# Kernel optimization log

Measured on AMD Instinct MI355X. Metric: run time of the kernel, lower is better.

## Reference

```python
import jax, jax.numpy as jnp
import numpy as np

# Config: b=2, n=1024, dim=512, heads=8, dim_head=64, L=8 slices/head, temperature=0.1

def setup_inputs() -> dict:
    key = jax.random.key(0)
    ks = jax.random.split(key, 5)
    b, n, dim = 2, 1024, 512
    heads, dim_head, L = 8, 64, 8
    inner = heads * dim_head
    x = jax.random.normal(ks[0], (b, n, dim), jnp.float32)
    W_qkv = jax.random.normal(ks[1], (dim, 3 * inner), jnp.float32) * 0.02
    theta = jax.random.normal(ks[2], (heads, L, dim_head), jnp.float32)
    W_out = jax.random.normal(ks[3], (inner, dim), jnp.float32) * 0.02
    b_out = jnp.zeros((dim,), jnp.float32)
    return {"x": x, "W_qkv": W_qkv, "theta": theta, "W_out": W_out, "b_out": b_out}


def reference(x, W_qkv, theta, W_out, b_out):
    b, n, dim = x.shape
    heads, L, dim_head = theta.shape
    scale = dim_head ** -0.5
    temperature = 0.1
    # QKV projection (no bias) and head split: b n (h d) -> b h n d
    qkv = x @ W_qkv
    q, k, v = jnp.split(qkv, 3, axis=-1)
    sh = lambda t: t.reshape(b, n, heads, dim_head).transpose(0, 2, 1, 3)
    q = sh(q) * scale
    k = sh(k) * scale
    v = sh(v)
    # Esp: learnable unit slice directions per head, 1D projections
    th = theta / jnp.linalg.norm(theta, axis=-1, keepdims=True)  # [h, L, d]
    qp = jnp.einsum('bhnd,hld->bhln', q, th)  # [b,h,L,n]
    kp = jnp.einsum('bhnd,hld->bhln', k, th)
    # per-slice soft 1D transport plan (rows sum to 1), averaged over slices,
    # scaled to total-mass-1 plan (rows sum 1/n)
    d2 = (qp[..., :, None] - kp[..., None, :]) ** 2  # [b,h,L,n,n]
    plans = jax.nn.softmax(-d2 / temperature, axis=-1)
    P = plans.mean(axis=2) / n  # [b,h,n,n], rows sum to 1/n
    # SA: attn = attn * attn.shape[-1] -> row-stochastic
    attn = P * n
    out = jnp.einsum('bhnm,bhmd->bhnd', attn, v)
    out = out.transpose(0, 2, 1, 3).reshape(b, n, heads * dim_head)
    out = out @ W_out + b_out  # to_out Linear (dropout=0 in eval)
    return out, attn
```

## Files before the change

### kernel.cpp

```cpp
#include <hip/hip_runtime.h>
#include <hip/hip_bf16.h>

#define CEXP (-14.4269504088896340736f)

typedef __attribute__((ext_vector_type(8))) short bfrag8;
typedef __attribute__((ext_vector_type(4))) float fvec4;
typedef __attribute__((ext_vector_type(8))) unsigned short ushort8;

__device__ inline unsigned short f2bf(float f) {
    unsigned u = __builtin_bit_cast(unsigned, f);
    u += 0x7fffu + ((u >> 16) & 1u);
    return (unsigned short)(u >> 16);
}
__device__ inline float bf2f(unsigned short h) {
    unsigned u = ((unsigned)h) << 16;
    return __builtin_bit_cast(float, u);
}

template <int CTRL, int RMASK>
__device__ __forceinline__ float dpp_add(float v) {
    int m = __builtin_amdgcn_update_dpp(0, __builtin_bit_cast(int, v), CTRL, RMASK, 0xf, true);
    return v + __builtin_bit_cast(float, m);
}
__device__ __forceinline__ float wave_sum64(float v) {
    v = dpp_add<0xB1,  0xf>(v);
    v = dpp_add<0x4E,  0xf>(v);
    v = dpp_add<0x141, 0xf>(v);
    v = dpp_add<0x140, 0xf>(v);
    v = dpp_add<0x142, 0xa>(v);
    v = dpp_add<0x143, 0xc>(v);
    return __builtin_bit_cast(float, __builtin_amdgcn_readlane(__builtin_bit_cast(int, v), 63));
}

__global__ __launch_bounds__(256) void k_wproj(const float* __restrict__ Wqkv,
                                               const float* __restrict__ theta,
                                               float* __restrict__ Wqp,
                                               float* __restrict__ Wkp,
                                               float* __restrict__ Wv) {
    __shared__ float th_s[64 * 65];
    int tid = threadIdx.x;
    int hl = tid & 63, cl = tid >> 6;
    #pragma unroll
    for (int i = 0; i < 16; ++i) {
        int r = cl * 16 + i;
        th_s[r * 65 + hl] = theta[r * 64 + hl];
    }
    __syncthreads();
    const float* ts = th_s + hl * 65;
    float ss = 0.f;
    #pragma unroll 8
    for (int d = 0; d < 64; ++d) ss = fmaf(ts[d], ts[d], ss);
    float inv = rsqrtf(ss);
    int c = blockIdx.x * 4 + cl;
    int h = hl >> 3;
    const float* wq = Wqkv + c * 1536 + h * 64;
    const float* wk = wq + 512;
    float aq = 0.f, ak = 0.f;
    #pragma unroll 4
    for (int d = 0; d < 64; ++d) {
        float tv = ts[d];
        aq = fmaf(wq[d], tv, aq);
        ak = fmaf(wk[d], tv, ak);
    }
    Wqp[c * 64 + hl] = aq * inv;
    Wkp[c * 64 + hl] = ak * inv;

    int c0 = blockIdx.x * 4;
    const float4* src = (const float4*)(Wqkv + 1024);
    float4* dst = (float4*)Wv;
    #pragma unroll
    for (int j = 0; j < 2; ++j) {
        int idx = j * 256 + tid;
        int cr = c0 + (idx >> 7), o4 = idx & 127;
        dst[cr * 128 + o4] = src[cr * 384 + o4];
    }
}

__global__ __launch_bounds__(512) void k_qkp(const float* __restrict__ x,
                                             const float* __restrict__ Wqp,
                                             const float* __restrict__ Wkp,
                                             float* __restrict__ qp,
                                             float* __restrict__ kp) {
    __shared__ float xs[4 * 512];
    __shared__ float comb[4][128][4];
    int tid = threadIdx.x;
    int i0 = blockIdx.x * 4;
    const float4* xg = (const float4*)(x + i0 * 512);
    ((float4*)xs)[tid] = xg[tid];
    __syncthreads();

    int t  = tid & 127;
    int kh = tid >> 7;
    int hl = t & 63;
    const float* Bm = (t & 64) ? Wkp : Wqp;
    float a[4] = {0.f, 0.f, 0.f, 0.f};
    int c4b = kh * 32;
    for (int c4 = c4b; c4 < c4b + 32; ++c4) {
        float b0 = Bm[(c4 * 4 + 0) * 64 + hl];
        float b1 = Bm[(c4 * 4 + 1) * 64 + hl];
        float b2 = Bm[(c4 * 4 + 2) * 64 + hl];
        float b3 = Bm[(c4 * 4 + 3) * 64 + hl];
        #pragma unroll
        for (int r = 0; r < 4; ++r) {
            float4 xv = *(const float4*)(xs + r * 512 + c4 * 4);
            a[r] = fmaf(xv.x, b0, fmaf(xv.y, b1, fmaf(xv.z, b2, fmaf(xv.w, b3, a[r]))));
        }
    }
    #pragma unroll
    for (int r = 0; r < 4; ++r) comb[kh][t][r] = a[r];
    __syncthreads();

    if (tid < 128) {
        int hl2 = tid & 63;
        int h = hl2 >> 3, l = hl2 & 7;
        float* dst = (tid & 64) ? kp : qp;
        int b = i0 >> 10, i = i0 & 1023;
        fvec4 st;
        #pragma unroll
        for (int r = 0; r < 4; ++r)
            st[r] = (comb[0][tid][r] + comb[1][tid][r] + comb[2][tid][r] + comb[3][tid][r]) * 0.125f;
        *(fvec4*)(dst + ((b * 8 + h) * 8 + l) * 1024 + i) = st;
    }
}

__global__ __launch_bounds__(256) void k_vproj(const float* __restrict__ x,
                                               const float* __restrict__ Wv,
                                               unsigned short* __restrict__ vThi,
                                               unsigned short* __restrict__ vTlo) {
    __shared__ float xs[8 * 512];
    __shared__ float comb[2][128][8];
    int tid = threadIdx.x;
    int blk = blockIdx.x;
    int cs = blk & 3;
    int i0 = (blk >> 2) * 8;
    const float4* xg = (const float4*)(x + i0 * 512);
    float4* xs4 = (float4*)xs;
    #pragma unroll
    for (int j = 0; j < 4; ++j) xs4[j * 256 + tid] = xg[j * 256 + tid];
    __syncthreads();

    int t  = tid & 127;
    int kh = tid >> 7;
    int col = cs * 128 + t;
    const float* wp = Wv + col;
    float a[8];
    #pragma unroll
    for (int r = 0; r < 8; ++r) a[r] = 0.f;
    int c4b = kh * 64;
    for (int c4 = c4b; c4 < c4b + 64; ++c4) {
        float w0 = wp[(c4 * 4 + 0) * 512];
        float w1 = wp[(c4 * 4 + 1) * 512];
        float w2 = wp[(c4 * 4 + 2) * 512];
        float w3 = wp[(c4 * 4 + 3) * 512];
        #pragma unroll
        for (int r = 0; r < 8; ++r) {
            float4 xv = *(const float4*)(xs + r * 512 + c4 * 4);
            a[r] = fmaf(xv.x, w0, fmaf(xv.y, w1, fmaf(xv.z, w2, fmaf(xv.w, w3, a[r]))));
        }
    }
    #pragma unroll
    for (int r = 0; r < 8; ++r) comb[kh][t][r] = a[r];
    __syncthreads();

    if (tid < 128) {
        int col2 = cs * 128 + tid;
        int h = col2 >> 6, d = col2 & 63;
        int b = i0 >> 10, ib = i0 & 1023;
        ushort8 vh, vl;
        #pragma unroll
        for (int r = 0; r < 8; ++r) {
            float v = comb[0][tid][r] + comb[1][tid][r];
            unsigned short hi = f2bf(v);
            vh[r] = hi;
            vl[r] = f2bf(v - bf2f(hi));
        }
        size_t off = (size_t)(b * 8 + h) * 65536 + (size_t)d * 1024 + ib;
        *(ushort8*)(vThi + off) = vh;
        *(ushort8*)(vTlo + off) = vl;
    }
}

__global__ __launch_bounds__(512) void k_attn_pv(const float* __restrict__ qp,
                                                 const float* __restrict__ kp,
                                                 const unsigned short* __restrict__ vThi,
                                                 const unsigned short* __restrict__ vTlo,
                                                 float* __restrict__ attn,
                                                 float* __restrict__ oh) {
    __shared__ float s_buf[8 * 1024];
    __shared__ float sc[4 * 64 * 4];
    int bx = blockIdx.x;
    int idx = bx >> 3;
    int bh = (bx & 7) * 2 + (idx >> 7);
    int rowbase = (idx & 127) * 8;
    int tid = threadIdx.x;
    int w = tid >> 6, lane = tid & 63;

    const float4* kp4 = (const float4*)(kp + bh * 8192);
    float4* kps4 = (float4*)s_buf;
    #pragma unroll
    for (int k = 0; k < 4; ++k) kps4[k * 512 + tid] = kp4[k * 512 + tid];

    int r = rowbase + w;
    float qv[8];
    #pragma unroll
    for (int l = 0; l < 8; ++l) qv[l] = qp[bh * 8192 + l * 1024 + r];
    __syncthreads();

    const fvec4 CE = {CEXP, CEXP, CEXP, CEXP};
    fvec4 acc4[4];
    #pragma unroll
    for (int mm = 0; mm < 4; ++mm) acc4[mm] = (fvec4){0.f, 0.f, 0.f, 0.f};

    for (int l = 0; l < 8; ++l) {
        fvec4 kv4[4], e4[4];
        #pragma unroll
        for (int mm = 0; mm < 4; ++mm)
            kv4[mm] = *(const fvec4*)(s_buf + l * 1024 + mm * 256 + lane * 4);
        float sqs = -2.f * CEXP * qv[l];
        fvec4 sq4 = {sqs, sqs, sqs, sqs};
        fvec4 sum4 = {0.f, 0.f, 0.f, 0.f};
        #pragma unroll
        for (int mm = 0; mm < 4; ++mm) {
            fvec4 k2 = (kv4[mm] * kv4[mm]) * CE;
            fvec4 t  = sq4 * kv4[mm] + k2;
            fvec4 e;
            e[0] = __builtin_amdgcn_exp2f(t[0]);
            e[1] = __builtin_amdgcn_exp2f(t[1]);
            e[2] = __builtin_amdgcn_exp2f(t[2]);
            e[3] = __builtin_amdgcn_exp2f(t[3]);
            e4[mm] = e;
            sum4 += e;
        }
        float s = (sum4[0] + sum4[1]) + (sum4[2] + sum4[3]);
        float inv = 0.125f * __builtin_amdgcn_rcpf(wave_sum64(s));
        fvec4 inv4 = {inv, inv, inv, inv};
        #pragma unroll
        for (int mm = 0; mm < 4; ++mm) acc4[mm] = e4[mm] * inv4 + acc4[mm];
    }

    __syncthreads();

    unsigned short* ps = (unsigned short*)s_buf;
    int swz = w << 3;
    #pragma unroll
    for (int mm = 0; mm < 4; ++mm) {
        #pragma unroll
        for (int jj = 0; jj < 4; ++jj) {
            int j = mm * 256 + lane * 4 + jj;
            float v = acc4[mm][jj];
            unsigned short hi = f2bf(v);
            ps[w * 1024 + (j ^ swz)]       = hi;
            ps[(w + 8) * 1024 + (j ^ swz)] = f2bf(v - bf2f(hi));
        }
    }
    __syncthreads();

    float* aR = attn + ((size_t)(bh * 1024 + r)) * 1024;
    #pragma unroll
    for (int mm = 0; mm < 4; ++mm)
        __builtin_nontemporal_store(acc4[mm], (fvec4*)(aR + mm * 256 + lane * 4));

    int n0 = (w & 3) * 16;
    int kh = w >> 2;
    int ar  = lane & 15;
    int asw = (ar & 7) << 3;
    int ak  = (lane >> 4) * 8;
    const unsigned short* ap = ps + ar * 1024;
    size_t boff = (size_t)bh * 65536 + (size_t)(n0 + (lane & 15)) * 1024 + ak;
    const unsigned short* bh_p = vThi + boff;
    const unsigned short* bl_p = vTlo + boff;
    fvec4 c2 = {0.f, 0.f, 0.f, 0.f};
    #pragma unroll 4
    for (int s = kh * 16; s < kh * 16 + 16; ++s) {
        bfrag8 a  = *(const bfrag8*)(ap + ((s * 32 + ak) ^ asw));
        bfrag8 vh = *(const bfrag8*)(bh_p + s * 32);
        bfrag8 vl = *(const bfrag8*)(bl_p + s * 32);
        c2 = __builtin_amdgcn_mfma_f32_16x16x32_bf16(a, vh, c2, 0, 0, 0);
        c2 = __builtin_amdgcn_mfma_f32_16x16x32_bf16(a, vl, c2, 0, 0, 0);
    }
    if (w >= 4) {
        #pragma unroll
        for (int q = 0; q < 4; ++q) sc[(w - 4) * 256 + lane * 4 + q] = c2[q];
    }
    __syncthreads();
    if (w < 4) {
        int b = bh >> 3, h = bh & 7;
        #pragma unroll
        for (int q = 0; q < 4; ++q) {
            float t = c2[q] + sc[w * 256 + lane * 4 + q];
            t += __shfl_xor(t, 32);
            if (lane < 32) {
                int row = rowbase + (lane >> 4) * 4 + q;
                oh[(b * 1024 + row) * 512 + h * 64 + n0 + (lane & 15)] = t;
            }
        }
    }
}

__global__ __launch_bounds__(256) void k_out(const float* __restrict__ oh,
                                             const float* __restrict__ Wout,
                                             const float* __restrict__ bout,
                                             float* __restrict__ out) {
    __shared__ float xs[8 * 512];
    __shared__ float comb[2][128][8];
    int tid = threadIdx.x;
    int blk = blockIdx.x;
    int cs = blk & 3;
    int i0 = (blk >> 2) * 8;
    const float4* xg = (const float4*)(oh + i0 * 512);
    float4* xs4 = (float4*)xs;
    #pragma unroll
    for (int j = 0; j < 4; ++j) xs4[j * 256 + tid] = xg[j * 256 + tid];
    __syncthreads();

    int t  = tid & 127;
    int kh = tid >> 7;
    int col = cs * 128 + t;
    const float* wp = Wout + col;
    float a[8];
    #pragma unroll
    for (int r = 0; r < 8; ++r) a[r] = 0.f;
    int c4b = kh * 64;
    for (int c4 = c4b; c4 < c4b + 64; ++c4) {
        float w0 = wp[(c4 * 4 + 0) * 512];
        float w1 = wp[(c4 * 4 + 1) * 512];
        float w2 = wp[(c4 * 4 + 2) * 512];
        float w3 = wp[(c4 * 4 + 3) * 512];
        #pragma unroll
        for (int r = 0; r < 8; ++r) {
            float4 xv = *(const float4*)(xs + r * 512 + c4 * 4);
            a[r] = fmaf(xv.x, w0, fmaf(xv.y, w1, fmaf(xv.z, w2, fmaf(xv.w, w3, a[r]))));
        }
    }
    #pragma unroll
    for (int r = 0; r < 8; ++r) comb[kh][t][r] = a[r];
    __syncthreads();

    if (tid < 128) {
        int col2 = cs * 128 + tid;
        float bias = bout[col2];
        #pragma unroll
        for (int r = 0; r < 8; ++r)
            out[(i0 + r) * 512 + col2] = comb[0][tid][r] + comb[1][tid][r] + bias;
    }
}

extern "C" void kernel_launch(void* const* d_in, const int* in_sizes, int n_in,
                              void* d_out, int out_size, void* d_ws, size_t ws_size,
                              hipStream_t stream) {
    const float* x     = (const float*)d_in[0];
    const float* Wqkv  = (const float*)d_in[1];
    const float* theta = (const float*)d_in[2];
    const float* Wout  = (const float*)d_in[3];
    const float* bout  = (const float*)d_in[4];

    float* out  = (float*)d_out;
    float* attn = out + 2 * 1024 * 512;

    float* ws  = (float*)d_ws;
    float* Wqp = ws;
    float* Wkp = ws + 32768;
    float* qp  = ws + 65536;
    float* kp  = ws + 196608;
    unsigned short* vThi = (unsigned short*)(ws + 327680);
    unsigned short* vTlo = (unsigned short*)(ws + 851968);
    float* oh   = ws + 1376256;
    float* Wv   = ws + 2424832;

    k_wproj   <<<128,  256, 0, stream>>>(Wqkv, theta, Wqp, Wkp, Wv);
    k_qkp     <<<512,  512, 0, stream>>>(x, Wqp, Wkp, qp, kp);
    k_vproj   <<<1024, 256, 0, stream>>>(x, Wv, vThi, vTlo);
    k_attn_pv <<<2048, 512, 0, stream>>>(qp, kp, vThi, vTlo, attn, oh);
    k_out     <<<1024, 256, 0, stream>>>(oh, Wout, bout, out);
}
```

Measured before the change: 138.1 us.

## Move output projection to split-bf16 MFMA with pre-transposed W_out

```diff
diff --git a/kernel.cpp b/kernel.cpp
--- a/kernel.cpp
+++ b/kernel.cpp
@@ -6,6 +6,7 @@
 typedef __attribute__((ext_vector_type(8))) short bfrag8;
 typedef __attribute__((ext_vector_type(4))) float fvec4;
 typedef __attribute__((ext_vector_type(8))) unsigned short ushort8;
+typedef __attribute__((ext_vector_type(4))) unsigned short ushort4v;
 
 __device__ inline unsigned short f2bf(float f) {
     unsigned u = __builtin_bit_cast(unsigned, f);
@@ -34,10 +35,14 @@
 
 __global__ __launch_bounds__(256) void k_wproj(const float* __restrict__ Wqkv,
                                                const float* __restrict__ theta,
+                                               const float* __restrict__ Wout,
                                                float* __restrict__ Wqp,
                                                float* __restrict__ Wkp,
-                                               float* __restrict__ Wv) {
+                                               float* __restrict__ Wv,
+                                               unsigned short* __restrict__ WoThi,
+                                               unsigned short* __restrict__ WoTlo) {
     __shared__ float th_s[64 * 65];
+    __shared__ float ts2[64 * 65];
     int tid = threadIdx.x;
     int hl = tid & 63, cl = tid >> 6;
     #pragma unroll
@@ -65,14 +70,35 @@
     Wqp[c * 64 + hl] = aq * inv;
     Wkp[c * 64 + hl] = ak * inv;
 
-    int c0 = blockIdx.x * 4;
+    int c0b = blockIdx.x * 4;
     const float4* src = (const float4*)(Wqkv + 1024);
     float4* dst = (float4*)Wv;
     #pragma unroll
     for (int j = 0; j < 2; ++j) {
         int idx = j * 256 + tid;
-        int cr = c0 + (idx >> 7), o4 = idx & 127;
+        int cr = c0b + (idx >> 7), o4 = idx & 127;
         dst[cr * 128 + o4] = src[cr * 384 + o4];
+    }
+
+    if (blockIdx.x < 64) {
+        int r0 = (blockIdx.x >> 3) * 64;
+        int c0 = (blockIdx.x & 7) * 64;
+        int cc = tid & 63, rr = tid >> 6;
+        #pragma unroll
+        for (int k = 0; k < 16; ++k) {
+            int r = rr + 4 * k;
+            ts2[r * 65 + cc] = Wout[(r0 + r) * 512 + c0 + cc];
+        }
+        __syncthreads();
+        int kk = tid & 63, nn = tid >> 6;
+        #pragma unroll
+        for (int i = 0; i < 16; ++i) {
+            int n = nn + 4 * i;
+            float v = ts2[kk * 65 + n];
+            unsigned short hi = f2bf(v);
+            WoThi[(size_t)(c0 + n) * 512 + r0 + kk] = hi;
+            WoTlo[(size_t)(c0 + n) * 512 + r0 + kk] = f2bf(v - bf2f(hi));
+        }
     }
 }
 
@@ -113,13 +139,13 @@
     if (tid < 128) {
         int hl2 = tid & 63;
         int h = hl2 >> 3, l = hl2 & 7;
-        float* dst = (tid & 64) ? kp : qp;
+        float* dstp = (tid & 64) ? kp : qp;
         int b = i0 >> 10, i = i0 & 1023;
         fvec4 st;
         #pragma unroll
         for (int r = 0; r < 4; ++r)
             st[r] = (comb[0][tid][r] + comb[1][tid][r] + comb[2][tid][r] + comb[3][tid][r]) * 0.125f;
-        *(fvec4*)(dst + ((b * 8 + h) * 8 + l) * 1024 + i) = st;
+        *(fvec4*)(dstp + ((b * 8 + h) * 8 + l) * 1024 + i) = st;
     }
 }
 
@@ -206,7 +232,7 @@
     for (int l = 0; l < 8; ++l) qv[l] = qp[bh * 8192 + l * 1024 + r];
     __syncthreads();
 
-    const fvec4 CE = {CEXP, CEXP, CEXP, CEXP};
+    const fvec4 CE4 = {CEXP, CEXP, CEXP, CEXP};
     fvec4 acc4[4];
     #pragma unroll
     for (int mm = 0; mm < 4; ++mm) acc4[mm] = (fvec4){0.f, 0.f, 0.f, 0.f};
@@ -221,7 +247,7 @@
         fvec4 sum4 = {0.f, 0.f, 0.f, 0.f};
         #pragma unroll
         for (int mm = 0; mm < 4; ++mm) {
-            fvec4 k2 = (kv4[mm] * kv4[mm]) * CE;
+            fvec4 k2 = (kv4[mm] * kv4[mm]) * CE4;
             fvec4 t  = sq4 * kv4[mm] + k2;
             fvec4 e;
             e[0] = __builtin_amdgcn_exp2f(t[0]);
@@ -244,14 +270,17 @@
     int swz = w << 3;
     #pragma unroll
     for (int mm = 0; mm < 4; ++mm) {
+        ushort4v h4, l4;
         #pragma unroll
         for (int jj = 0; jj < 4; ++jj) {
-            int j = mm * 256 + lane * 4 + jj;
             float v = acc4[mm][jj];
             unsigned short hi = f2bf(v);
-            ps[w * 1024 + (j ^ swz)]       = hi;
-            ps[(w + 8) * 1024 + (j ^ swz)] = f2bf(v - bf2f(hi));
-        }
+            h4[jj] = hi;
+            l4[jj] = f2bf(v - bf2f(hi));
+        }
+        int j0 = mm * 256 + lane * 4;
+        *(ushort4v*)(ps + w * 1024 + (j0 ^ swz))       = h4;
+        *(ushort4v*)(ps + (w + 8) * 1024 + (j0 ^ swz)) = l4;
     }
     __syncthreads();
 
@@ -298,50 +327,71 @@
 }
 
 __global__ __launch_bounds__(256) void k_out(const float* __restrict__ oh,
-                                             const float* __restrict__ Wout,
+                                             const unsigned short* __restrict__ WoThi,
+                                             const unsigned short* __restrict__ WoTlo,
                                              const float* __restrict__ bout,
                                              float* __restrict__ out) {
-    __shared__ float xs[8 * 512];
-    __shared__ float comb[2][128][8];
-    int tid = threadIdx.x;
+    __shared__ unsigned short ps[32 * 512];
     int blk = blockIdx.x;
     int cs = blk & 3;
-    int i0 = (blk >> 2) * 8;
-    const float4* xg = (const float4*)(oh + i0 * 512);
-    float4* xs4 = (float4*)xs;
-    #pragma unroll
-    for (int j = 0; j < 4; ++j) xs4[j * 256 + tid] = xg[j * 256 + tid];
-    __syncthreads();
-
-    int t  = tid & 127;
-    int kh = tid >> 7;
-    int col = cs * 128 + t;
-    const float* wp = Wout + col;
-    float a[8];
-    #pragma unroll
-    for (int r = 0; r < 8; ++r) a[r] = 0.f;
-    int c4b = kh * 64;
-    for (int c4 = c4b; c4 < c4b + 64; ++c4) {
-        float w0 = wp[(c4 * 4 + 0) * 512];
-        float w1 = wp[(c4 * 4 + 1) * 512];
-        float w2 = wp[(c4 * 4 + 2) * 512];
-        float w3 = wp[(c4 * 4 + 3) * 512];
-        #pragma unroll
-        for (int r = 0; r < 8; ++r) {
-            float4 xv = *(const float4*)(xs + r * 512 + c4 * 4);
-            a[r] = fmaf(xv.x, w0, fmaf(xv.y, w1, fmaf(xv.z, w2, fmaf(xv.w, w3, a[r]))));
-        }
-    }
-    #pragma unroll
-    for (int r = 0; r < 8; ++r) comb[kh][t][r] = a[r];
-    __syncthreads();
-
-    if (tid < 128) {
-        int col2 = cs * 128 + tid;
-        float bias = bout[col2];
-        #pragma unroll
-        for (int r = 0; r < 8; ++r)
-            out[(i0 + r) * 512 + col2] = comb[0][tid][r] + comb[1][tid][r] + bias;
+    int rg = blk >> 2;
+    int tid = threadIdx.x;
+    int w = tid >> 6, lane = tid & 63;
+
+    const float4* og = (const float4*)(oh + (size_t)rg * 16 * 512);
+    #pragma unroll
+    for (int rep = 0; rep < 8; ++rep) {
+        int idx = rep * 256 + tid;
+        int row = idx >> 7, c4 = idx & 127;
+        float4 v = og[idx];
+        int swz = (row & 7) << 3;
+        int cbase = c4 * 4;
+        ushort4v h4, l4;
+        float vv[4] = {v.x, v.y, v.z, v.w};
+        #pragma unroll
+        for (int jj = 0; jj < 4; ++jj) {
+            unsigned short hi = f2bf(vv[jj]);
+            h4[jj] = hi;
+            l4[jj] = f2bf(vv[jj] - bf2f(hi));
+        }
+        *(ushort4v*)(ps + row * 512 + (cbase ^ swz))        = h4;
+        *(ushort4v*)(ps + (row + 16) * 512 + (cbase ^ swz)) = l4;
+    }
+    __syncthreads();
+
+    int ar  = lane & 15;
+    int asw = (ar & 7) << 3;
+    int ak  = (lane >> 4) * 8;
+    const unsigned short* aph = ps + ar * 512;
+    const unsigned short* apl = ps + (ar + 16) * 512;
+    int colb = cs * 128 + w * 32;
+    size_t b0 = (size_t)(colb + ar) * 512 + ak;
+    size_t b1 = b0 + 16 * 512;
+    fvec4 acc0 = {0.f, 0.f, 0.f, 0.f};
+    fvec4 acc1 = {0.f, 0.f, 0.f, 0.f};
+    #pragma unroll 4
+    for (int s = 0; s < 16; ++s) {
+        int ko = s * 32 + ak;
+        bfrag8 ahi = *(const bfrag8*)(aph + (ko ^ asw));
+        bfrag8 alo = *(const bfrag8*)(apl + (ko ^ asw));
+        bfrag8 bh0 = *(const bfrag8*)(WoThi + b0 + s * 32);
+        bfrag8 bl0 = *(const bfrag8*)(WoTlo + b0 + s * 32);
+        bfrag8 bh1 = *(const bfrag8*)(WoThi + b1 + s * 32);
+        bfrag8 bl1 = *(const bfrag8*)(WoTlo + b1 + s * 32);
+        acc0 = __builtin_amdgcn_mfma_f32_16x16x32_bf16(ahi, bh0, acc0, 0, 0, 0);
+        acc0 = __builtin_amdgcn_mfma_f32_16x16x32_bf16(ahi, bl0, acc0, 0, 0, 0);
+        acc0 = __builtin_amdgcn_mfma_f32_16x16x32_bf16(alo, bh0, acc0, 0, 0, 0);
+        acc1 = __builtin_amdgcn_mfma_f32_16x16x32_bf16(ahi, bh1, acc1, 0, 0, 0);
+        acc1 = __builtin_amdgcn_mfma_f32_16x16x32_bf16(ahi, bl1, acc1, 0, 0, 0);
+        acc1 = __builtin_amdgcn_mfma_f32_16x16x32_bf16(alo, bh1, acc1, 0, 0, 0);
+    }
+    int rowb = rg * 16 + (lane >> 4) * 4;
+    int col0 = colb + ar;
+    float bias0 = bout[col0], bias1 = bout[col0 + 16];
+    #pragma unroll
+    for (int q = 0; q < 4; ++q) {
+        out[(rowb + q) * 512 + col0]      = acc0[q] + bias0;
+        out[(rowb + q) * 512 + col0 + 16] = acc1[q] + bias1;
     }
 }
 
@@ -366,10 +416,12 @@
     unsigned short* vTlo = (unsigned short*)(ws + 851968);
     float* oh   = ws + 1376256;
     float* Wv   = ws + 2424832;
-
-    k_wproj   <<<128,  256, 0, stream>>>(Wqkv, theta, Wqp, Wkp, Wv);
+    unsigned short* WoThi = (unsigned short*)(ws + 2686976);
+    unsigned short* WoTlo = (unsigned short*)(ws + 2818048);
+
+    k_wproj   <<<128,  256, 0, stream>>>(Wqkv, theta, Wout, Wqp, Wkp, Wv, WoThi, WoTlo);
     k_qkp     <<<512,  512, 0, stream>>>(x, Wqp, Wkp, qp, kp);
     k_vproj   <<<1024, 256, 0, stream>>>(x, Wv, vThi, vTlo);
     k_attn_pv <<<2048, 512, 0, stream>>>(qp, kp, vThi, vTlo, attn, oh);
-    k_out     <<<1024, 256, 0, stream>>>(oh, Wout, bout, out);
-}
+    k_out     <<<512,  256, 0, stream>>>(oh, WoThi, WoTlo, bout, out);
+}
```

Measured after the change: 132.9 us. 3.7% less time.
